# Optimization experiments

Hardware: AMD Instinct MI355X
Metric: run time of the kernel (lower is better)

Reference implementation:

```python
import jax, jax.numpy as jnp
import numpy as np

PI = float(np.pi)
N_BINS_POT = 140
TIMESTEP = 0.02
ATOMS = ["N", "CA", "C", "cent"]
ANGLES = [("N", "CA", "C", 0), ("CA", "C", "N", 1), ("C", "N", "CA", 2), ("N", "CA", "cent", 0), ("C", "CA", "cent", 0)]
DIHEDRALS = [("C", "N", "CA", "C", 3), ("N", "CA", "C", "N", 1), ("CA", "C", "N", "CA", 2), ("C", "N", "CA", "cent", 3), ("cent", "CA", "C", "N", 1)]

_gap_ang = (PI - PI / 3) / N_BINS_POT
ANGLE_CENTRES = np.array([PI / 3 + i * _gap_ang + 0.5 * _gap_ang for i in range(N_BINS_POT)][1:-1], dtype=np.float32)  # 138
_gap_dih = 2 * PI / N_BINS_POT
DIH_CENTRES = np.array([-PI + i * _gap_dih - 0.5 * _gap_dih for i in range(N_BINS_POT + 2)][1:-1], dtype=np.float32)  # 140


def safe_norm(v, axis=-1, keepdims=False):
    sq = jnp.sum(v * v, axis=axis, keepdims=keepdims)
    return jnp.where(sq > 0, jnp.sqrt(jnp.where(sq > 0, sq, 1.0)), 0.0)


def normalize(v):
    # torch.nn.functional.normalize with eps=1e-12
    return v / jnp.maximum(safe_norm(v, keepdims=True), 1e-12)


def _gather_force(pots, inds):
    # pots: [n, n_bins]; inds: [b, n] -> 0.5 * (pots[r, i] - pots[r, i+2])
    r = jnp.arange(pots.shape[0])[None, :]
    return 0.5 * (pots[r, inds] - pots[r, inds + 2])


def _accelerations(coords, masses, pair_centres, pair_pots, angle_pots, dih_pots):
    b, n_atoms, _ = coords.shape
    n_res = n_atoms // 4
    # ---- all-pairs distance forces (bin by argmin against per-pair centres, gather) ----
    diffs = coords[:, None, :, :] - coords[:, :, None, :]  # [b, i, j, 3] = c[j] - c[i]
    dists = safe_norm(diffs)  # [b, i, j]
    df = dists.reshape(b, n_atoms * n_atoms)
    inds = jnp.argmin(jnp.abs(pair_centres[None] - df[:, :, None]), axis=2)  # [b, n^2]
    pair_forces = _gather_force(pair_pots, inds).reshape(b, n_atoms, n_atoms)
    norm_diffs = diffs / jnp.maximum(dists, 0.01)[..., None]
    accs = jnp.sum(pair_forces[..., None] * norm_diffs, axis=1) / masses[..., None]
    # ---- bond-angle forces ----
    ac = coords.reshape(b, n_res, 4, 3)
    aa = jnp.zeros_like(ac)
    ang_centres = jnp.asarray(ANGLE_CENTRES)
    for ai, (a1, a2, a3, across) in enumerate(ANGLES):
        i1, i2, i3 = ATOMS.index(a1), ATOMS.index(a2), ATOMS.index(a3)
        if across == 0:
            ba = ac[:, :, i1] - ac[:, :, i2]; bc = ac[:, :, i3] - ac[:, :, i2]; pots = angle_pots[ai]
        elif across == 1:
            ba = ac[:, :-1, i1] - ac[:, :-1, i2]; bc = ac[:, 1:, i3] - ac[:, :-1, i2]; pots = angle_pots[ai][:-1]
        else:
            ba = ac[:, :-1, i1] - ac[:, 1:, i2]; bc = ac[:, 1:, i3] - ac[:, 1:, i2]; pots = angle_pots[ai][1:]
        ban = safe_norm(ba); bcn = safe_norm(bc)
        angs = jnp.arccos(jnp.sum(ba * bc, axis=2) / (ban * bcn))
        ainds = jnp.argmin(jnp.abs(ang_centres[None, None] - angs[:, :, None]), axis=2)
        f = _gather_force(pots, ainds)[..., None]
        cr = jnp.cross(ba, bc)
        fa = f * normalize(jnp.cross(ba, cr)) / ban[..., None]
        fc = f * normalize(jnp.cross(-bc, cr)) / bcn[..., None]
        fb = -fa - fc
        if across == 0:
            aa = aa.at[:, :, i1].add(fa).at[:, :, i2].add(fb).at[:, :, i3].add(fc)
        elif across == 1:
            aa = aa.at[:, :-1, i1].add(fa).at[:, :-1, i2].add(fb).at[:, 1:, i3].add(fc)
        else:
            aa = aa.at[:, :-1, i1].add(fa).at[:, 1:, i2].add(fb).at[:, 1:, i3].add(fc)
    # ---- dihedral forces ----
    dih_centres = jnp.asarray(DIH_CENTRES)
    for di, (a1, a2, a3, a4, across) in enumerate(DIHEDRALS):
        i1, i2, i3, i4 = ATOMS.index(a1), ATOMS.index(a2), ATOMS.index(a3), ATOMS.index(a4)
        if across == 1:
            ab = ac[:, :-1, i2] - ac[:, :-1, i1]; bc = ac[:, :-1, i3] - ac[:, :-1, i2]; cd = ac[:, 1:, i4] - ac[:, :-1, i3]
            pots = dih_pots[di][:-1]
        elif across == 2:
            ab = ac[:, :-1, i2] - ac[:, :-1, i1]; bc = ac[:, 1:, i3] - ac[:, :-1, i2]; cd = ac[:, 1:, i4] - ac[:, 1:, i3]
            pots = dih_pots[di][1:]
        else:  # across == 3
            ab = ac[:, 1:, i2] - ac[:, :-1, i1]; bc = ac[:, 1:, i3] - ac[:, 1:, i2]; cd = ac[:, 1:, i4] - ac[:, 1:, i3]
            pots = dih_pots[di][1:]
        c1 = jnp.cross(ab, bc); c2 = jnp.cross(bc, cd)
        bcn = safe_norm(bc, keepdims=True)
        dihs = jnp.arctan2(jnp.sum(jnp.cross(c1, c2) * bc / bcn, axis=2), jnp.sum(c1 * c2, axis=2))
        dinds = jnp.argmin(jnp.abs(dih_centres[None, None] - dihs[:, :, None]), axis=2)
        f = _gather_force(pots, dinds)[..., None]
        fa = f * normalize(-c1) / safe_norm(ab, keepdims=True)
        fd = f * normalize(c2) / safe_norm(cd, keepdims=True)
        bsq = jnp.squeeze(bcn, -1) ** 2
        t1 = (jnp.sum(ab * bc, axis=2) / bsq)[..., None]
        t2 = (jnp.sum(cd * bc, axis=2) / bsq)[..., None]
        fb = -fa - t1 * fa + t2 * fd  # torque-balancing middle-atom forces
        fc = -fa - fb - fd
        if across == 1:
            aa = aa.at[:, :-1, i1].add(fa).at[:, :-1, i2].add(fb).at[:, :-1, i3].add(fc).at[:, 1:, i4].add(fd)
        elif across == 2:
            aa = aa.at[:, :-1, i1].add(fa).at[:, :-1, i2].add(fb).at[:, 1:, i3].add(fc).at[:, 1:, i4].add(fd)
        else:
            aa = aa.at[:, :-1, i1].add(fa).at[:, 1:, i2].add(fb).at[:, 1:, i3].add(fc).at[:, 1:, i4].add(fd)
    return accs + aa.reshape(b, n_atoms, 3) / masses[..., None]


def _simulate(coords, vels, masses, ff_distances, ff_angles, ff_dihedrals,
              dist_bin_centres, inters_flat, inters_ang, inters_dih, n_steps):
    pair_centres = dist_bin_centres[inters_flat]  # [n^2, 138]
    pair_pots = ff_distances[inters_flat]         # [n^2, 140]
    angle_pots = ff_angles[:, inters_ang]         # [5, n_res, 140]
    dih_pots = ff_dihedrals[:, inters_dih]        # [5, n_res, 142]

    def step(carry, _):
        c, v, a_last = carry
        c = c + v * TIMESTEP + 0.5 * a_last * TIMESTEP * TIMESTEP
        a = _accelerations(c, masses, pair_centres, pair_pots, angle_pots, dih_pots)
        v = v + 0.5 * (a_last + a) * TIMESTEP
        return (c, v, a), None

    (coords, vels, _), _ = jax.lax.scan(step, (coords, vels, jnp.zeros_like(coords)), None, length=n_steps)
    return coords


def setup_inputs() -> dict:
    key = jax.random.key(0)
    ks = jax.random.split(key, 10)
    b, n_res = 1, 100
    n_atoms = n_res * 4
    n2 = n_atoms * n_atoms
    n_dist_types = 4000
    coords = jax.random.normal(ks[0], (b, n_atoms, 3), jnp.float32) * 10.0
    vels = jax.random.normal(ks[1], (b, n_atoms, 3), jnp.float32) * 0.1  # start_temperature = 0.1
    masses = jax.random.uniform(ks[2], (b, n_atoms), jnp.float32, 0.5, 1.5)
    native_coords = jax.random.normal(ks[3], (b, n_atoms, 3), jnp.float32) * 10.0
    ff_distances = jax.random.normal(ks[4], (n_dist_types, 140), jnp.float32) * 0.1
    ff_angles = jax.random.normal(ks[5], (5, 20, 140), jnp.float32) * 0.1
    ff_dihedrals = jax.random.normal(ks[6], (5, 20, 142), jnp.float32) * 0.1
    centres = jnp.linspace(1.0, 15.9, 138, dtype=jnp.float32)
    dist_bin_centres = jnp.tile(centres[None, :], (n_dist_types, 1))
    inters_flat = jax.random.randint(ks[7], (n2,), 0, n_dist_types)
    inters_ang = jax.random.randint(ks[8], (n_res,), 0, 20)
    inters_dih = jax.random.randint(ks[9], (n_res,), 0, 20)
    return {"coords": coords, "vels": vels, "masses": masses, "native_coords": native_coords,
            "ff_distances": ff_distances, "ff_angles": ff_angles, "ff_dihedrals": ff_dihedrals,
            "dist_bin_centres": dist_bin_centres, "inters_flat": inters_flat,
            "inters_ang": inters_ang, "inters_dih": inters_dih, "n_steps": 3}


def reference(coords, vels, masses, native_coords, ff_distances, ff_angles, ff_dihedrals,
              dist_bin_centres, inters_flat, inters_ang, inters_dih, n_steps):
    # native_coords is only used for RMSD reporting in the original; it does not affect the dynamics.
    return _simulate(coords, vels, masses, ff_distances, ff_angles, ff_dihedrals,
                     dist_bin_centres, inters_flat, inters_ang, inters_dih, n_steps)
```

## Files before the change

### kernel.cpp

```cpp
#include <hip/hip_runtime.h>
#include <math.h>

#define N_ATOMS 400
#define N_RES   100
#define DT      0.02f
#define PI_D    3.14159265358979323846

struct V3 { float x, y, z; };
__device__ __forceinline__ V3 v3(float x, float y, float z) { V3 r{x,y,z}; return r; }
__device__ __forceinline__ V3 sub(V3 a, V3 b) { return v3(a.x-b.x, a.y-b.y, a.z-b.z); }
__device__ __forceinline__ V3 neg(V3 a) { return v3(-a.x, -a.y, -a.z); }
__device__ __forceinline__ V3 scale(V3 a, float s) { return v3(a.x*s, a.y*s, a.z*s); }
__device__ __forceinline__ float dot3(V3 a, V3 b) { return a.x*b.x + a.y*b.y + a.z*b.z; }
__device__ __forceinline__ V3 cross3(V3 a, V3 b) {
    return v3(a.y*b.z - a.z*b.y, a.z*b.x - a.x*b.z, a.x*b.y - a.y*b.x);
}
__device__ __forceinline__ float vnorm(V3 a) {
    float s = dot3(a, a);
    return s > 0.0f ? sqrtf(s) : 0.0f;
}
__device__ __forceinline__ V3 normalize3(V3 a) {
    float n = fmaxf(vnorm(a), 1e-12f);
    return scale(a, 1.0f/n);
}

__device__ __forceinline__ int clampi(int i, int lo, int hi) {
    return i < lo ? lo : (i > hi ? hi : i);
}
__device__ __forceinline__ int bin_dist(float d) {
    const float INV = (float)(137.0/14.9);
    return clampi((int)floorf((d - 1.0f)*INV + 0.5f), 0, 137);
}
__device__ __forceinline__ int bin_ang(float a) {
    const float C0  = (float)(PI_D/3.0 + 1.5*((PI_D - PI_D/3.0)/140.0));
    const float INV = (float)(140.0/(PI_D - PI_D/3.0));
    return clampi((int)floorf((a - C0)*INV + 0.5f), 0, 137);
}
__device__ __forceinline__ int bin_dih(float a) {
    const float C0  = (float)(-PI_D + 0.5*(2.0*PI_D/140.0));
    const float INV = (float)(140.0/(2.0*PI_D));
    return clampi((int)floorf((a - C0)*INV + 0.5f), 0, 139);
}

__constant__ int ANG_I[5][3]   = {{0,1,2},{1,2,0},{2,0,1},{0,1,3},{2,1,3}};
__constant__ int ANG_ACROSS[5] = {0,1,2,0,0};
__constant__ int DIH_I[5][4]   = {{2,0,1,2},{0,1,2,0},{1,2,0,1},{2,0,1,3},{3,1,2,0}};
__constant__ int DIH_ACROSS[5] = {3,1,2,3,1};

__device__ __forceinline__ V3 ldpos(const float* c, int res, int atom) {
    int b = (res*4 + atom)*3;
    return v3(c[b], c[b+1], c[b+2]);
}
__device__ __forceinline__ void addF(float* F, int res, int atom, V3 f) {
    int b = (res*4 + atom)*3;
    atomicAdd(&F[b],   f.x);
    atomicAdd(&F[b+1], f.y);
    atomicAdd(&F[b+2], f.z);
}

__global__ void init_kernel(const float* __restrict__ c_in, const float* __restrict__ v_in,
                            float* __restrict__ c, float* __restrict__ v, float* __restrict__ al) {
    int t = blockIdx.x*blockDim.x + threadIdx.x;
    if (t < N_ATOMS*3) { c[t] = c_in[t]; v[t] = v_in[t]; al[t] = 0.0f; }
}

__global__ void pos_kernel(float* __restrict__ c, const float* __restrict__ v,
                           const float* __restrict__ al, float* __restrict__ out) {
    int t = blockIdx.x*blockDim.x + threadIdx.x;
    if (t < N_ATOMS*3) {
        float cc = c[t] + v[t]*DT + 0.5f*al[t]*DT*DT;
        c[t] = cc;
        if (out) out[t] = cc;
    }
}

__global__ void pair_kernel(const float* __restrict__ c, const int* __restrict__ iflat,
                            const float* __restrict__ ffd, float* __restrict__ F) {
    int j = blockIdx.x;
    float cx = c[3*j], cy = c[3*j+1], cz = c[3*j+2];
    float fx = 0.0f, fy = 0.0f, fz = 0.0f;
    for (int i = threadIdx.x; i < N_ATOMS; i += 64) {
        float dx = cx - c[3*i];
        float dy = cy - c[3*i+1];
        float dz = cz - c[3*i+2];
        float d2 = dx*dx + dy*dy + dz*dz;
        float d  = d2 > 0.0f ? sqrtf(d2) : 0.0f;
        int ind  = bin_dist(d);
        int type = iflat[i*N_ATOMS + j];
        const float* row = ffd + (long)type*140;
        float f = 0.5f*(row[ind] - row[ind+2]);
        float w = f / fmaxf(d, 0.01f);
        fx += w*dx; fy += w*dy; fz += w*dz;
    }
    #pragma unroll
    for (int off = 32; off > 0; off >>= 1) {
        fx += __shfl_down(fx, off);
        fy += __shfl_down(fy, off);
        fz += __shfl_down(fz, off);
    }
    if (threadIdx.x == 0) { F[3*j] = fx; F[3*j+1] = fy; F[3*j+2] = fz; }
}

__global__ void bonded_kernel(const float* __restrict__ c, const float* __restrict__ ffa,
                              const float* __restrict__ ffdih, const int* __restrict__ ia,
                              const int* __restrict__ idh, float* __restrict__ F) {
    int t = blockIdx.x*blockDim.x + threadIdx.x;
    if (t < 500) {
        int ai = t/100, r = t%100;
        int across = ANG_ACROSS[ai];
        if (across != 0 && r >= N_RES-1) return;
        int i1 = ANG_I[ai][0], i2 = ANG_I[ai][1], i3 = ANG_I[ai][2];
        int o2 = (across == 2) ? 1 : 0;
        int o3 = (across != 0) ? 1 : 0;
        V3 p1 = ldpos(c, r,     i1);
        V3 p2 = ldpos(c, r+o2,  i2);
        V3 p3 = ldpos(c, r+o3,  i3);
        V3 ba = sub(p1, p2);
        V3 bc = sub(p3, p2);
        float ban = vnorm(ba), bcn = vnorm(bc);
        float ca = dot3(ba, bc) / (ban*bcn);
        ca = fminf(1.0f, fmaxf(-1.0f, ca));
        float ang = acosf(ca);
        int ind = bin_ang(ang);
        int potr = (across == 2) ? r+1 : r;
        const float* row = ffa + (ai*20 + ia[potr])*140;
        float f = 0.5f*(row[ind] - row[ind+2]);
        V3 cr = cross3(ba, bc);
        V3 fa = scale(normalize3(cross3(ba, cr)), f/ban);
        V3 fc = scale(normalize3(neg(cross3(bc, cr))), f/bcn);
        V3 fb = neg(v3(fa.x+fc.x, fa.y+fc.y, fa.z+fc.z));
        addF(F, r,     i1, fa);
        addF(F, r+o2,  i2, fb);
        addF(F, r+o3,  i3, fc);
    } else if (t < 500 + 5*(N_RES-1)) {
        int u = t - 500;
        int di = u/(N_RES-1), r = u%(N_RES-1);
        int across = DIH_ACROSS[di];
        int i1 = DIH_I[di][0], i2 = DIH_I[di][1], i3 = DIH_I[di][2], i4 = DIH_I[di][3];
        int o2 = (across == 3) ? 1 : 0;
        int o3 = (across >= 2) ? 1 : 0;
        int o4 = 1;
        V3 p1 = ldpos(c, r,     i1);
        V3 p2 = ldpos(c, r+o2,  i2);
        V3 p3 = ldpos(c, r+o3,  i3);
        V3 p4 = ldpos(c, r+o4,  i4);
        V3 ab = sub(p2, p1);
        V3 bc = sub(p3, p2);
        V3 cd = sub(p4, p3);
        V3 c1 = cross3(ab, bc);
        V3 c2 = cross3(bc, cd);
        float bcn = vnorm(bc);
        V3 cc = cross3(c1, c2);
        float y = dot3(cc, bc) / bcn;
        float x = dot3(c1, c2);
        float dih = atan2f(y, x);
        int ind = bin_dih(dih);
        int potr = (across == 1) ? r : r+1;
        const float* row = ffdih + (di*20 + idh[potr])*142;
        float f = 0.5f*(row[ind] - row[ind+2]);
        V3 fa = scale(normalize3(neg(c1)), f / vnorm(ab));
        V3 fd = scale(normalize3(c2),      f / vnorm(cd));
        float bsq = bcn*bcn;
        float t1 = dot3(ab, bc)/bsq;
        float t2 = dot3(cd, bc)/bsq;
        V3 fb = v3(-fa.x - t1*fa.x + t2*fd.x,
                   -fa.y - t1*fa.y + t2*fd.y,
                   -fa.z - t1*fa.z + t2*fd.z);
        V3 fc = v3(-fa.x - fb.x - fd.x,
                   -fa.y - fb.y - fd.y,
                   -fa.z - fb.z - fd.z);
        addF(F, r,     i1, fa);
        addF(F, r+o2,  i2, fb);
        addF(F, r+o3,  i3, fc);
        addF(F, r+o4,  i4, fd);
    }
}

__global__ void vel_kernel(const float* __restrict__ F, const float* __restrict__ masses,
                           float* __restrict__ v, float* __restrict__ al) {
    int t = blockIdx.x*blockDim.x + threadIdx.x;
    if (t < N_ATOMS*3) {
        int atom = t/3;
        float a = F[t] / masses[atom];
        v[t] += 0.5f*(al[t] + a)*DT;
        al[t] = a;
    }
}

extern "C" void kernel_launch(void* const* d_in, const int* in_sizes, int n_in,
                              void* d_out, int out_size, void* d_ws, size_t ws_size,
                              hipStream_t stream) {
    const float* coords = (const float*)d_in[0];
    const float* vels   = (const float*)d_in[1];
    const float* masses = (const float*)d_in[2];
    const float* ffd    = (const float*)d_in[4];
    const float* ffa    = (const float*)d_in[5];
    const float* ffdih  = (const float*)d_in[6];
    const int* iflat    = (const int*)d_in[8];
    const int* ia       = (const int*)d_in[9];
    const int* idh      = (const int*)d_in[10];
    float* out = (float*)d_out;

    float* ws = (float*)d_ws;
    float* c  = ws;
    float* v  = ws + 1200;
    float* al = ws + 2400;
    float* F  = ws + 3600;

    init_kernel<<<5, 256, 0, stream>>>(coords, vels, c, v, al);
    const int N_STEPS = 3;
    for (int s = 0; s < N_STEPS; ++s) {
        pos_kernel<<<5, 256, 0, stream>>>(c, v, al, (s == N_STEPS-1) ? out : nullptr);
        if (s < N_STEPS-1) {
            pair_kernel<<<N_ATOMS, 64, 0, stream>>>(c, iflat, ffd, F);
            bonded_kernel<<<4, 256, 0, stream>>>(c, ffa, ffdih, ia, idh, F);
            vel_kernel<<<5, 256, 0, stream>>>(F, masses, v, al);
        }
    }
}
```

Baseline: 111.1 us.

## Fuse whole simulation into one cooperative persistent kernel with grid syncs

Replaces the chain of about nine small kernel launches with a single cooperative kernel of 100 blocks. Grid-wide syncs separate the force, velocity and position phases, and coordinates are staged in shared memory for the pair and bonded computations. Pair and bonded forces go into separate buffers, and the velocity and position updates are merged into one step. This targets launch overhead, at the cost of grid-sync latency and a dependency on cooperative launch support, with the old multi-kernel path kept as a fallback.

```diff
diff --git a/kernel.cpp b/kernel.cpp
--- a/kernel.cpp
+++ b/kernel.cpp
@@ -1,10 +1,15 @@
 #include <hip/hip_runtime.h>
+#include <hip/hip_cooperative_groups.h>
 #include <math.h>
+
+namespace cg = cooperative_groups;
 
 #define N_ATOMS 400
 #define N_RES   100
 #define DT      0.02f
 #define PI_D    3.14159265358979323846
+#define NBLK    100
+#define NTHR    256
 
 struct V3 { float x, y, z; };
 __device__ __forceinline__ V3 v3(float x, float y, float z) { V3 r{x,y,z}; return r; }
@@ -58,80 +63,38 @@
     atomicAdd(&F[b+2], f.z);
 }
 
-__global__ void init_kernel(const float* __restrict__ c_in, const float* __restrict__ v_in,
-                            float* __restrict__ c, float* __restrict__ v, float* __restrict__ al) {
-    int t = blockIdx.x*blockDim.x + threadIdx.x;
-    if (t < N_ATOMS*3) { c[t] = c_in[t]; v[t] = v_in[t]; al[t] = 0.0f; }
-}
-
-__global__ void pos_kernel(float* __restrict__ c, const float* __restrict__ v,
-                           const float* __restrict__ al, float* __restrict__ out) {
-    int t = blockIdx.x*blockDim.x + threadIdx.x;
-    if (t < N_ATOMS*3) {
-        float cc = c[t] + v[t]*DT + 0.5f*al[t]*DT*DT;
-        c[t] = cc;
-        if (out) out[t] = cc;
-    }
-}
-
-__global__ void pair_kernel(const float* __restrict__ c, const int* __restrict__ iflat,
-                            const float* __restrict__ ffd, float* __restrict__ F) {
-    int j = blockIdx.x;
-    float cx = c[3*j], cy = c[3*j+1], cz = c[3*j+2];
-    float fx = 0.0f, fy = 0.0f, fz = 0.0f;
-    for (int i = threadIdx.x; i < N_ATOMS; i += 64) {
-        float dx = cx - c[3*i];
-        float dy = cy - c[3*i+1];
-        float dz = cz - c[3*i+2];
-        float d2 = dx*dx + dy*dy + dz*dz;
-        float d  = d2 > 0.0f ? sqrtf(d2) : 0.0f;
-        int ind  = bin_dist(d);
-        int type = iflat[i*N_ATOMS + j];
-        const float* row = ffd + (long)type*140;
-        float f = 0.5f*(row[ind] - row[ind+2]);
-        float w = f / fmaxf(d, 0.01f);
-        fx += w*dx; fy += w*dy; fz += w*dz;
-    }
-    #pragma unroll
-    for (int off = 32; off > 0; off >>= 1) {
-        fx += __shfl_down(fx, off);
-        fy += __shfl_down(fy, off);
-        fz += __shfl_down(fz, off);
-    }
-    if (threadIdx.x == 0) { F[3*j] = fx; F[3*j+1] = fy; F[3*j+2] = fz; }
-}
-
-__global__ void bonded_kernel(const float* __restrict__ c, const float* __restrict__ ffa,
-                              const float* __restrict__ ffdih, const int* __restrict__ ia,
-                              const int* __restrict__ idh, float* __restrict__ F) {
-    int t = blockIdx.x*blockDim.x + threadIdx.x;
+__device__ __forceinline__ void bonded_item(int t, const float* c,
+                              const float* __restrict__ ffa, const float* __restrict__ ffdih,
+                              const int* __restrict__ ia, const int* __restrict__ idh,
+                              float* __restrict__ Fb) {
     if (t < 500) {
         int ai = t/100, r = t%100;
         int across = ANG_ACROSS[ai];
-        if (across != 0 && r >= N_RES-1) return;
-        int i1 = ANG_I[ai][0], i2 = ANG_I[ai][1], i3 = ANG_I[ai][2];
-        int o2 = (across == 2) ? 1 : 0;
-        int o3 = (across != 0) ? 1 : 0;
-        V3 p1 = ldpos(c, r,     i1);
-        V3 p2 = ldpos(c, r+o2,  i2);
-        V3 p3 = ldpos(c, r+o3,  i3);
-        V3 ba = sub(p1, p2);
-        V3 bc = sub(p3, p2);
-        float ban = vnorm(ba), bcn = vnorm(bc);
-        float ca = dot3(ba, bc) / (ban*bcn);
-        ca = fminf(1.0f, fmaxf(-1.0f, ca));
-        float ang = acosf(ca);
-        int ind = bin_ang(ang);
-        int potr = (across == 2) ? r+1 : r;
-        const float* row = ffa + (ai*20 + ia[potr])*140;
-        float f = 0.5f*(row[ind] - row[ind+2]);
-        V3 cr = cross3(ba, bc);
-        V3 fa = scale(normalize3(cross3(ba, cr)), f/ban);
-        V3 fc = scale(normalize3(neg(cross3(bc, cr))), f/bcn);
-        V3 fb = neg(v3(fa.x+fc.x, fa.y+fc.y, fa.z+fc.z));
-        addF(F, r,     i1, fa);
-        addF(F, r+o2,  i2, fb);
-        addF(F, r+o3,  i3, fc);
+        if (across == 0 || r < N_RES-1) {
+            int i1 = ANG_I[ai][0], i2 = ANG_I[ai][1], i3 = ANG_I[ai][2];
+            int o2 = (across == 2) ? 1 : 0;
+            int o3 = (across != 0) ? 1 : 0;
+            V3 p1 = ldpos(c, r,     i1);
+            V3 p2 = ldpos(c, r+o2,  i2);
+            V3 p3 = ldpos(c, r+o3,  i3);
+            V3 ba = sub(p1, p2);
+            V3 bc = sub(p3, p2);
+            float ban = vnorm(ba), bcn = vnorm(bc);
+            float ca = dot3(ba, bc) / (ban*bcn);
+            ca = fminf(1.0f, fmaxf(-1.0f, ca));
+            float ang = acosf(ca);
+            int ind = bin_ang(ang);
+            int potr = (across == 2) ? r+1 : r;
+            const float* row = ffa + (ai*20 + ia[potr])*140;
+            float f = 0.5f*(row[ind] - row[ind+2]);
+            V3 cr = cross3(ba, bc);
+            V3 fa = scale(normalize3(cross3(ba, cr)), f/ban);
+            V3 fc = scale(normalize3(neg(cross3(bc, cr))), f/bcn);
+            V3 fb = neg(v3(fa.x+fc.x, fa.y+fc.y, fa.z+fc.z));
+            addF(Fb, r,     i1, fa);
+            addF(Fb, r+o2,  i2, fb);
+            addF(Fb, r+o3,  i3, fc);
+        }
     } else if (t < 500 + 5*(N_RES-1)) {
         int u = t - 500;
         int di = u/(N_RES-1), r = u%(N_RES-1);
@@ -169,11 +132,143 @@
         V3 fc = v3(-fa.x - fb.x - fd.x,
                    -fa.y - fb.y - fd.y,
                    -fa.z - fb.z - fd.z);
-        addF(F, r,     i1, fa);
-        addF(F, r+o2,  i2, fb);
-        addF(F, r+o3,  i3, fc);
-        addF(F, r+o4,  i4, fd);
-    }
+        addF(Fb, r,     i1, fa);
+        addF(Fb, r+o2,  i2, fb);
+        addF(Fb, r+o3,  i3, fc);
+        addF(Fb, r+o4,  i4, fd);
+    }
+}
+
+__global__ void __launch_bounds__(NTHR)
+sim_kernel(const float* __restrict__ cin, const float* __restrict__ vin,
+           const float* __restrict__ masses, const float* __restrict__ ffd,
+           const float* __restrict__ ffa, const float* __restrict__ ffdih,
+           const int* __restrict__ iflat, const int* __restrict__ ia,
+           const int* __restrict__ idh, float* __restrict__ out,
+           float* __restrict__ c, float* __restrict__ v, float* __restrict__ al,
+           float* __restrict__ Fp, float* __restrict__ Fb)
+{
+    cg::grid_group grid = cg::this_grid();
+    __shared__ float sc[N_ATOMS*3];
+    const int tid  = threadIdx.x;
+    const int b    = blockIdx.x;
+    const int g    = b*NTHR + tid;
+    const int lane = tid & 63;
+    const int wave = tid >> 6;
+    const int j    = b*4 + wave;
+
+    if (tid < 12) {
+        int t = b*12 + tid;
+        float vv = vin[t];
+        c[t]  = cin[t] + vv*DT;
+        v[t]  = vv;
+        al[t] = 0.0f;
+        Fb[t] = 0.0f;
+    }
+    __threadfence();
+    grid.sync();
+
+    for (int s = 0; s < 2; ++s) {
+        for (int t = tid; t < N_ATOMS*3; t += NTHR) sc[t] = c[t];
+        __syncthreads();
+
+        bonded_item(g, sc, ffa, ffdih, ia, idh, Fb);
+
+        float cx = sc[3*j], cy = sc[3*j+1], cz = sc[3*j+2];
+        float fx = 0.0f, fy = 0.0f, fz = 0.0f;
+        #pragma unroll
+        for (int k = 0; k < 7; ++k) {
+            int i = lane + 64*k;
+            if (i < N_ATOMS) {
+                float dx = cx - sc[3*i];
+                float dy = cy - sc[3*i+1];
+                float dz = cz - sc[3*i+2];
+                float d2 = dx*dx + dy*dy + dz*dz;
+                float d  = d2 > 0.0f ? sqrtf(d2) : 0.0f;
+                int ind  = bin_dist(d);
+                int type = iflat[i*N_ATOMS + j];
+                const float* row = ffd + type*140;
+                float f = 0.5f*(row[ind] - row[ind+2]);
+                float w = f / fmaxf(d, 0.01f);
+                fx += w*dx; fy += w*dy; fz += w*dz;
+            }
+        }
+        #pragma unroll
+        for (int off = 32; off > 0; off >>= 1) {
+            fx += __shfl_down(fx, off);
+            fy += __shfl_down(fy, off);
+            fz += __shfl_down(fz, off);
+        }
+        if (lane == 0) { Fp[3*j] = fx; Fp[3*j+1] = fy; Fp[3*j+2] = fz; }
+        __threadfence();
+        grid.sync();
+
+        if (tid < 12) {
+            int t = b*12 + tid;
+            float a  = (Fp[t] + Fb[t]) / masses[t/3];
+            float vv = v[t] + 0.5f*(al[t] + a)*DT;
+            v[t]  = vv;
+            al[t] = a;
+            Fb[t] = 0.0f;
+            float ccur = c[t] + vv*DT + 0.5f*a*DT*DT;
+            c[t] = ccur;
+            if (s == 1) out[t] = ccur;
+        }
+        if (s == 0) {
+            __threadfence();
+            grid.sync();
+        }
+    }
+}
+
+__global__ void init_kernel(const float* __restrict__ c_in, const float* __restrict__ v_in,
+                            float* __restrict__ c, float* __restrict__ v, float* __restrict__ al) {
+    int t = blockIdx.x*blockDim.x + threadIdx.x;
+    if (t < N_ATOMS*3) { c[t] = c_in[t]; v[t] = v_in[t]; al[t] = 0.0f; }
+}
+
+__global__ void pos_kernel(float* __restrict__ c, const float* __restrict__ v,
+                           const float* __restrict__ al, float* __restrict__ out) {
+    int t = blockIdx.x*blockDim.x + threadIdx.x;
+    if (t < N_ATOMS*3) {
+        float cc = c[t] + v[t]*DT + 0.5f*al[t]*DT*DT;
+        c[t] = cc;
+        if (out) out[t] = cc;
+    }
+}
+
+__global__ void pair_kernel(const float* __restrict__ c, const int* __restrict__ iflat,
+                            const float* __restrict__ ffd, float* __restrict__ F) {
+    int j = blockIdx.x;
+    float cx = c[3*j], cy = c[3*j+1], cz = c[3*j+2];
+    float fx = 0.0f, fy = 0.0f, fz = 0.0f;
+    for (int i = threadIdx.x; i < N_ATOMS; i += 64) {
+        float dx = cx - c[3*i];
+        float dy = cy - c[3*i+1];
+        float dz = cz - c[3*i+2];
+        float d2 = dx*dx + dy*dy + dz*dz;
+        float d  = d2 > 0.0f ? sqrtf(d2) : 0.0f;
+        int ind  = bin_dist(d);
+        int type = iflat[i*N_ATOMS + j];
+        const float* row = ffd + type*140;
+        float f = 0.5f*(row[ind] - row[ind+2]);
+        float w = f / fmaxf(d, 0.01f);
+        fx += w*dx; fy += w*dy; fz += w*dz;
+    }
+    #pragma unroll
+    for (int off = 32; off > 0; off >>= 1) {
+        fx += __shfl_down(fx, off);
+        fy += __shfl_down(fy, off);
+        fz += __shfl_down(fz, off);
+    }
+    if (threadIdx.x == 0) { F[3*j] = fx; F[3*j+1] = fy; F[3*j+2] = fz; }
+}
+
+__global__ void bonded_kernel(const float* __restrict__ c, const float* __restrict__ ffa,
+                              const float* __restrict__ ffdih, const int* __restrict__ ia,
+                              const int* __restrict__ idh, float* __restrict__ F) {
+    int t = blockIdx.x*blockDim.x + threadIdx.x;
+    if (t < 995) bonded_item(t, c, ffa, ffdih, ia, idh, F);
 }
 
 __global__ void vel_kernel(const float* __restrict__ F, const float* __restrict__ masses,
@@ -205,16 +300,29 @@
     float* c  = ws;
     float* v  = ws + 1200;
     float* al = ws + 2400;
-    float* F  = ws + 3600;
-
-    init_kernel<<<5, 256, 0, stream>>>(coords, vels, c, v, al);
-    const int N_STEPS = 3;
-    for (int s = 0; s < N_STEPS; ++s) {
-        pos_kernel<<<5, 256, 0, stream>>>(c, v, al, (s == N_STEPS-1) ? out : nullptr);
-        if (s < N_STEPS-1) {
-            pair_kernel<<<N_ATOMS, 64, 0, stream>>>(c, iflat, ffd, F);
-            bonded_kernel<<<4, 256, 0, stream>>>(c, ffa, ffdih, ia, idh, F);
-            vel_kernel<<<5, 256, 0, stream>>>(F, masses, v, al);
-        }
-    }
-}
+    float* Fp = ws + 3600;
+    float* Fb = ws + 4800;
+
+    void* args[] = {
+        (void*)&coords, (void*)&vels, (void*)&masses, (void*)&ffd,
+        (void*)&ffa, (void*)&ffdih, (void*)&iflat, (void*)&ia,
+        (void*)&idh, (void*)&out, (void*)&c, (void*)&v,
+        (void*)&al, (void*)&Fp, (void*)&Fb
+    };
+    hipError_t err = hipLaunchCooperativeKernel((const void*)sim_kernel,
+                                                dim3(NBLK), dim3(NTHR),
+                                                args, 0, stream);
+    if (err != hipSuccess) {
+        float* F = Fp;
+        init_kernel<<<5, 256, 0, stream>>>(coords, vels, c, v, al);
+        const int N_STEPS = 3;
+        for (int s = 0; s < N_STEPS; ++s) {
+            pos_kernel<<<5, 256, 0, stream>>>(c, v, al, (s == N_STEPS-1) ? out : nullptr);
+            if (s < N_STEPS-1) {
+                pair_kernel<<<N_ATOMS, 64, 0, stream>>>(c, iflat, ffd, F);
+                bonded_kernel<<<4, 256, 0, stream>>>(c, ffa, ffdih, ia, idh, F);
+                vel_kernel<<<5, 256, 0, stream>>>(F, masses, v, al);
+            }
+        }
+    }
+}
```

After: 201.3 us. 1.81x slower.

## Fuse all simulation steps into one persistent kernel with a grid barrier

Applied to the files above, without the earlier changes.

Replaces the chain of init/pos/pair/bonded/vel launches (about ten kernels) with one init kernel and one persistent 100-block kernel. Each block owns one residue, stages the coordinates in shared memory, computes pair and bonded forces for its own four atoms without global atomics, and does the velocity and position update in registers. A spin-wait grid barrier on a global counter separates the two force steps. This removes kernel launch overhead and global round trips, but relies on all 100 blocks being co-resident and has a bounded spin that could break silently.

```diff
diff --git a/kernel.cpp b/kernel.cpp
--- a/kernel.cpp
+++ b/kernel.cpp
@@ -5,6 +5,8 @@
 #define N_RES   100
 #define DT      0.02f
 #define PI_D    3.14159265358979323846
+#define NBLK    100
+#define NTHR    256
 
 struct V3 { float x, y, z; };
 __device__ __forceinline__ V3 v3(float x, float y, float z) { V3 r{x,y,z}; return r; }
@@ -48,73 +50,35 @@
 __constant__ int DIH_ACROSS[5] = {3,1,2,3,1};
 
 __device__ __forceinline__ V3 ldpos(const float* c, int res, int atom) {
-    int b = (res*4 + atom)*3;
-    return v3(c[b], c[b+1], c[b+2]);
-}
-__device__ __forceinline__ void addF(float* F, int res, int atom, V3 f) {
-    int b = (res*4 + atom)*3;
-    atomicAdd(&F[b],   f.x);
-    atomicAdd(&F[b+1], f.y);
-    atomicAdd(&F[b+2], f.z);
-}
-
-__global__ void init_kernel(const float* __restrict__ c_in, const float* __restrict__ v_in,
-                            float* __restrict__ c, float* __restrict__ v, float* __restrict__ al) {
-    int t = blockIdx.x*blockDim.x + threadIdx.x;
-    if (t < N_ATOMS*3) { c[t] = c_in[t]; v[t] = v_in[t]; al[t] = 0.0f; }
-}
-
-__global__ void pos_kernel(float* __restrict__ c, const float* __restrict__ v,
-                           const float* __restrict__ al, float* __restrict__ out) {
-    int t = blockIdx.x*blockDim.x + threadIdx.x;
-    if (t < N_ATOMS*3) {
-        float cc = c[t] + v[t]*DT + 0.5f*al[t]*DT*DT;
-        c[t] = cc;
-        if (out) out[t] = cc;
-    }
-}
-
-__global__ void pair_kernel(const float* __restrict__ c, const int* __restrict__ iflat,
-                            const float* __restrict__ ffd, float* __restrict__ F) {
-    int j = blockIdx.x;
-    float cx = c[3*j], cy = c[3*j+1], cz = c[3*j+2];
-    float fx = 0.0f, fy = 0.0f, fz = 0.0f;
-    for (int i = threadIdx.x; i < N_ATOMS; i += 64) {
-        float dx = cx - c[3*i];
-        float dy = cy - c[3*i+1];
-        float dz = cz - c[3*i+2];
-        float d2 = dx*dx + dy*dy + dz*dz;
-        float d  = d2 > 0.0f ? sqrtf(d2) : 0.0f;
-        int ind  = bin_dist(d);
-        int type = iflat[i*N_ATOMS + j];
-        const float* row = ffd + (long)type*140;
-        float f = 0.5f*(row[ind] - row[ind+2]);
-        float w = f / fmaxf(d, 0.01f);
-        fx += w*dx; fy += w*dy; fz += w*dz;
-    }
-    #pragma unroll
-    for (int off = 32; off > 0; off >>= 1) {
-        fx += __shfl_down(fx, off);
-        fy += __shfl_down(fy, off);
-        fz += __shfl_down(fz, off);
-    }
-    if (threadIdx.x == 0) { F[3*j] = fx; F[3*j+1] = fy; F[3*j+2] = fz; }
-}
-
-__global__ void bonded_kernel(const float* __restrict__ c, const float* __restrict__ ffa,
-                              const float* __restrict__ ffdih, const int* __restrict__ ia,
-                              const int* __restrict__ idh, float* __restrict__ F) {
-    int t = blockIdx.x*blockDim.x + threadIdx.x;
-    if (t < 500) {
-        int ai = t/100, r = t%100;
-        int across = ANG_ACROSS[ai];
-        if (across != 0 && r >= N_RES-1) return;
-        int i1 = ANG_I[ai][0], i2 = ANG_I[ai][1], i3 = ANG_I[ai][2];
+    int k = (res*4 + atom)*3;
+    return v3(c[k], c[k+1], c[k+2]);
+}
+
+__device__ __forceinline__ void addOwn(float* sF, int b, int res, int atom, V3 f) {
+    if (res == b) {
+        atomicAdd(&sF[atom*3+0], f.x);
+        atomicAdd(&sF[atom*3+1], f.y);
+        atomicAdd(&sF[atom*3+2], f.z);
+    }
+}
+
+__device__ __forceinline__ void bonded_own(int u, int b, const float* sc,
+                              const float* __restrict__ ffa, const float* __restrict__ ffdih,
+                              const int* __restrict__ ia, const int* __restrict__ idh,
+                              float* sF) {
+    int e = u % 10, which = u / 10;
+    int r = b - which;
+    if (e < 5) {
+        int across = ANG_ACROSS[e];
+        bool valid = which ? (b >= 1 && across != 0)
+                           : (across == 0 || b <= N_RES-2);
+        if (!valid) return;
+        int i1 = ANG_I[e][0], i2 = ANG_I[e][1], i3 = ANG_I[e][2];
         int o2 = (across == 2) ? 1 : 0;
         int o3 = (across != 0) ? 1 : 0;
-        V3 p1 = ldpos(c, r,     i1);
-        V3 p2 = ldpos(c, r+o2,  i2);
-        V3 p3 = ldpos(c, r+o3,  i3);
+        V3 p1 = ldpos(sc, r,     i1);
+        V3 p2 = ldpos(sc, r+o2,  i2);
+        V3 p3 = ldpos(sc, r+o3,  i3);
         V3 ba = sub(p1, p2);
         V3 bc = sub(p3, p2);
         float ban = vnorm(ba), bcn = vnorm(bc);
@@ -123,27 +87,28 @@
         float ang = acosf(ca);
         int ind = bin_ang(ang);
         int potr = (across == 2) ? r+1 : r;
-        const float* row = ffa + (ai*20 + ia[potr])*140;
+        const float* row = ffa + (e*20 + ia[potr])*140;
         float f = 0.5f*(row[ind] - row[ind+2]);
         V3 cr = cross3(ba, bc);
         V3 fa = scale(normalize3(cross3(ba, cr)), f/ban);
         V3 fc = scale(normalize3(neg(cross3(bc, cr))), f/bcn);
         V3 fb = neg(v3(fa.x+fc.x, fa.y+fc.y, fa.z+fc.z));
-        addF(F, r,     i1, fa);
-        addF(F, r+o2,  i2, fb);
-        addF(F, r+o3,  i3, fc);
-    } else if (t < 500 + 5*(N_RES-1)) {
-        int u = t - 500;
-        int di = u/(N_RES-1), r = u%(N_RES-1);
+        addOwn(sF, b, r,     i1, fa);
+        addOwn(sF, b, r+o2,  i2, fb);
+        addOwn(sF, b, r+o3,  i3, fc);
+    } else {
+        int di = e - 5;
+        bool valid = which ? (b >= 1) : (b <= N_RES-2);
+        if (!valid) return;
         int across = DIH_ACROSS[di];
         int i1 = DIH_I[di][0], i2 = DIH_I[di][1], i3 = DIH_I[di][2], i4 = DIH_I[di][3];
         int o2 = (across == 3) ? 1 : 0;
         int o3 = (across >= 2) ? 1 : 0;
         int o4 = 1;
-        V3 p1 = ldpos(c, r,     i1);
-        V3 p2 = ldpos(c, r+o2,  i2);
-        V3 p3 = ldpos(c, r+o3,  i3);
-        V3 p4 = ldpos(c, r+o4,  i4);
+        V3 p1 = ldpos(sc, r,     i1);
+        V3 p2 = ldpos(sc, r+o2,  i2);
+        V3 p3 = ldpos(sc, r+o3,  i3);
+        V3 p4 = ldpos(sc, r+o4,  i4);
         V3 ab = sub(p2, p1);
         V3 bc = sub(p3, p2);
         V3 cd = sub(p4, p3);
@@ -169,21 +134,104 @@
         V3 fc = v3(-fa.x - fb.x - fd.x,
                    -fa.y - fb.y - fd.y,
                    -fa.z - fb.z - fd.z);
-        addF(F, r,     i1, fa);
-        addF(F, r+o2,  i2, fb);
-        addF(F, r+o3,  i3, fc);
-        addF(F, r+o4,  i4, fd);
-    }
-}
-
-__global__ void vel_kernel(const float* __restrict__ F, const float* __restrict__ masses,
-                           float* __restrict__ v, float* __restrict__ al) {
+        addOwn(sF, b, r,     i1, fa);
+        addOwn(sF, b, r+o2,  i2, fb);
+        addOwn(sF, b, r+o3,  i3, fc);
+        addOwn(sF, b, r+o4,  i4, fd);
+    }
+}
+
+__device__ __forceinline__ void grid_barrier(int* bar) {
+    __syncthreads();
+    if (threadIdx.x == 0) {
+        __hip_atomic_fetch_add(bar, 1, __ATOMIC_RELEASE, __HIP_MEMORY_SCOPE_AGENT);
+        int iters = 0;
+        while (__hip_atomic_load(bar, __ATOMIC_RELAXED, __HIP_MEMORY_SCOPE_AGENT) < NBLK) {
+            __builtin_amdgcn_s_sleep(1);
+            if (++iters > (1 << 24)) break;
+        }
+        (void)__hip_atomic_load(bar, __ATOMIC_ACQUIRE, __HIP_MEMORY_SCOPE_AGENT);
+    }
+    __syncthreads();
+}
+
+__global__ void init_kernel(const float* __restrict__ cin, const float* __restrict__ vin,
+                            float* __restrict__ c, int* __restrict__ bar) {
     int t = blockIdx.x*blockDim.x + threadIdx.x;
-    if (t < N_ATOMS*3) {
-        int atom = t/3;
-        float a = F[t] / masses[atom];
-        v[t] += 0.5f*(al[t] + a)*DT;
-        al[t] = a;
+    if (t < N_ATOMS*3) c[t] = cin[t] + vin[t]*DT;
+    if (t < 4) bar[t] = 0;
+}
+
+__global__ void __launch_bounds__(NTHR)
+sim_kernel(const float* __restrict__ vin, const float* __restrict__ masses,
+           const float* __restrict__ ffd, const float* __restrict__ ffa,
+           const float* __restrict__ ffdih, const int* __restrict__ iflat,
+           const int* __restrict__ ia, const int* __restrict__ idh,
+           float* __restrict__ out, float* __restrict__ c, int* __restrict__ bar)
+{
+    __shared__ float sc[N_ATOMS*3];
+    __shared__ float sF[12];
+    const int tid  = threadIdx.x;
+    const int b    = blockIdx.x;
+    const int lane = tid & 63;
+    const int wave = tid >> 6;
+    const int j    = b*4 + wave;
+
+    float vv = 0.0f, aa = 0.0f;
+    if (tid < 12) vv = vin[b*12 + tid];
+
+    for (int s = 0; s < 2; ++s) {
+        for (int t = tid; t < N_ATOMS*3; t += NTHR)
+            sc[t] = __hip_atomic_load(&c[t], __ATOMIC_RELAXED, __HIP_MEMORY_SCOPE_AGENT);
+        if (tid < 12) sF[tid] = 0.0f;
+        __syncthreads();
+
+        if (tid < 20) bonded_own(tid, b, sc, ffa, ffdih, ia, idh, sF);
+
+        float cx = sc[3*j], cy = sc[3*j+1], cz = sc[3*j+2];
+        float fx = 0.0f, fy = 0.0f, fz = 0.0f;
+        #pragma unroll
+        for (int k = 0; k < 7; ++k) {
+            int i = lane + 64*k;
+            if (k < 6 || i < N_ATOMS) {
+                float dx = cx - sc[3*i];
+                float dy = cy - sc[3*i+1];
+                float dz = cz - sc[3*i+2];
+                float d2 = dx*dx + dy*dy + dz*dz;
+                float d  = d2 > 0.0f ? sqrtf(d2) : 0.0f;
+                int ind  = bin_dist(d);
+                int type = iflat[i*N_ATOMS + j];
+                const float* row = ffd + type*140;
+                float f = 0.5f*(row[ind] - row[ind+2]);
+                float w = f / fmaxf(d, 0.01f);
+                fx += w*dx; fy += w*dy; fz += w*dz;
+            }
+        }
+        #pragma unroll
+        for (int off = 32; off > 0; off >>= 1) {
+            fx += __shfl_down(fx, off);
+            fy += __shfl_down(fy, off);
+            fz += __shfl_down(fz, off);
+        }
+        if (lane == 0) {
+            atomicAdd(&sF[wave*3+0], fx);
+            atomicAdd(&sF[wave*3+1], fy);
+            atomicAdd(&sF[wave*3+2], fz);
+        }
+        __syncthreads();
+
+        if (tid < 12) {
+            int t = b*12 + tid;
+            float a = sF[tid] / masses[b*4 + tid/3];
+            vv += 0.5f*(aa + a)*DT;
+            aa = a;
+            float cc = sc[t] + vv*DT + 0.5f*a*DT*DT;
+            if (s == 0)
+                __hip_atomic_store(&c[t], cc, __ATOMIC_RELAXED, __HIP_MEMORY_SCOPE_AGENT);
+            else
+                out[t] = cc;
+        }
+        if (s == 0) grid_barrier(bar);
     }
 }
 
@@ -201,20 +249,11 @@
     const int* idh      = (const int*)d_in[10];
     float* out = (float*)d_out;
 
-    float* ws = (float*)d_ws;
-    float* c  = ws;
-    float* v  = ws + 1200;
-    float* al = ws + 2400;
-    float* F  = ws + 3600;
-
-    init_kernel<<<5, 256, 0, stream>>>(coords, vels, c, v, al);
-    const int N_STEPS = 3;
-    for (int s = 0; s < N_STEPS; ++s) {
-        pos_kernel<<<5, 256, 0, stream>>>(c, v, al, (s == N_STEPS-1) ? out : nullptr);
-        if (s < N_STEPS-1) {
-            pair_kernel<<<N_ATOMS, 64, 0, stream>>>(c, iflat, ffd, F);
-            bonded_kernel<<<4, 256, 0, stream>>>(c, ffa, ffdih, ia, idh, F);
-            vel_kernel<<<5, 256, 0, stream>>>(F, masses, v, al);
-        }
-    }
-}
+    float* ws  = (float*)d_ws;
+    float* c   = ws;
+    int*   bar = (int*)(ws + 1200);
+
+    init_kernel<<<5, 256, 0, stream>>>(coords, vels, c, bar);
+    sim_kernel<<<NBLK, NTHR, 0, stream>>>(vels, masses, ffd, ffa, ffdih,
+                                          iflat, ia, idh, out, c, bar);
+}
```

After: 98.47 us. 1.13x faster.
